# Kernel optimization log

Measured on AMD Instinct MI355X. Metric: run time of the kernel, lower is better.

Reference implementation:

```python
import jax, jax.numpy as jnp
import numpy as np
from jax import lax

ITER = 10
SMOOTH = 1.0


def _max_pool3(x):
    # 3x3 max pool, stride 1, pad 1 (torch pads with -inf for max pool)
    return lax.reduce_window(x, -np.inf, lax.max,
                             window_dimensions=(1, 1, 3, 3),
                             window_strides=(1, 1, 1, 1),
                             padding=((0, 0), (0, 0), (1, 1), (1, 1)))


def soft_skeletonize(x, thresh_width=ITER):
    def body(i, x):
        min_pool_x = -_max_pool3(-x)
        contour = jax.nn.relu(_max_pool3(min_pool_x) - min_pool_x)
        return jax.nn.relu(x - contour)
    return lax.fori_loop(0, thresh_width, body, x)


def setup_inputs() -> dict:
    key = jax.random.key(0)
    k1, k2 = jax.random.split(key)
    shape = (32, 2, 512, 512)
    y_pred = jax.random.uniform(k1, shape, dtype=jnp.float32)
    y_true = jax.random.uniform(k2, shape, dtype=jnp.float32)
    return {"y_pred": y_pred, "y_true": y_true}


def reference(y_pred, y_true):
    skel_pred = soft_skeletonize(y_pred, ITER)
    skel_true = soft_skeletonize(y_true, ITER)
    tprec = (jnp.sum((skel_pred * y_true)[:, 1:]) + SMOOTH) / (jnp.sum(skel_pred[:, 1:]) + SMOOTH)
    tsens = (jnp.sum((skel_true * y_pred)[:, 1:]) + SMOOTH) / (jnp.sum(skel_true[:, 1:]) + SMOOTH)
    cl_dice = 1.0 - 2.0 * (tprec * tsens) / (tprec + tsens)
    return cl_dice
```

## Files before the change

kernel.cpp:

```cpp
#include <hip/hip_runtime.h>

#define IMG 512
#define HW (IMG * IMG)
#define NB 32
#define NIMG 64
#define BAND 32
#define NBAND (IMG / BAND)
#define NSTG 5
#define HALO (2 * NSTG)
#define T0OFF 20
#define NSTEP 36
#define INF __builtin_inff()

static __device__ __forceinline__ float dpp_from_prev(float v, float ident) {
    return __int_as_float(__builtin_amdgcn_update_dpp(
        __float_as_int(ident), __float_as_int(v), 0x138, 0xF, 0xF, false));
}
static __device__ __forceinline__ float dpp_from_next(float v, float ident) {
    return __int_as_float(__builtin_amdgcn_update_dpp(
        __float_as_int(ident), __float_as_int(v), 0x130, 0xF, 0xF, false));
}

struct Row { float4 a, b; };

static __device__ __forceinline__ float min3f(float a, float b, float c) { return fminf(fminf(a, b), c); }
static __device__ __forceinline__ float max3f(float a, float b, float c) { return fmaxf(fmaxf(a, b), c); }

static __device__ __forceinline__ Row splat(float v) {
    Row r;
    r.a = make_float4(v, v, v, v);
    r.b = make_float4(v, v, v, v);
    return r;
}

static __device__ __forceinline__ Row rmin3(const Row& x, const Row& y, const Row& z) {
    Row o;
    const float* px = (const float*)&x;
    const float* py = (const float*)&y;
    const float* pz = (const float*)&z;
    float* po = (float*)&o;
#pragma unroll
    for (int i = 0; i < 8; ++i) po[i] = min3f(px[i], py[i], pz[i]);
    return o;
}

static __device__ __forceinline__ Row rmax3(const Row& x, const Row& y, const Row& z) {
    Row o;
    const float* px = (const float*)&x;
    const float* py = (const float*)&y;
    const float* pz = (const float*)&z;
    float* po = (float*)&o;
#pragma unroll
    for (int i = 0; i < 8; ++i) po[i] = max3f(px[i], py[i], pz[i]);
    return o;
}

static __device__ __forceinline__ Row hmin3(const Row& v) {
    float shl = dpp_from_prev(v.b.w, INF);
    float shr = dpp_from_next(v.a.x, INF);
    Row o;
    o.a.x = min3f(shl,   v.a.x, v.a.y);
    o.a.y = min3f(v.a.x, v.a.y, v.a.z);
    o.a.z = min3f(v.a.y, v.a.z, v.a.w);
    o.a.w = min3f(v.a.z, v.a.w, v.b.x);
    o.b.x = min3f(v.a.w, v.b.x, v.b.y);
    o.b.y = min3f(v.b.x, v.b.y, v.b.z);
    o.b.z = min3f(v.b.y, v.b.z, v.b.w);
    o.b.w = min3f(v.b.z, v.b.w, shr);
    return o;
}

static __device__ __forceinline__ Row hmax3(const Row& v) {
    float shl = dpp_from_prev(v.b.w, -INF);
    float shr = dpp_from_next(v.a.x, -INF);
    Row o;
    o.a.x = max3f(shl,   v.a.x, v.a.y);
    o.a.y = max3f(v.a.x, v.a.y, v.a.z);
    o.a.z = max3f(v.a.y, v.a.z, v.a.w);
    o.a.w = max3f(v.a.z, v.a.w, v.b.x);
    o.b.x = max3f(v.a.w, v.b.x, v.b.y);
    o.b.y = max3f(v.b.x, v.b.y, v.b.z);
    o.b.z = max3f(v.b.y, v.b.z, v.b.w);
    o.b.w = max3f(v.b.z, v.b.w, shr);
    return o;
}

static __device__ __forceinline__ Row relu_out(const Row& x, const Row& mp, const Row& mn) {
    Row o;
    const float* px = (const float*)&x;
    const float* pp = (const float*)&mp;
    const float* pm = (const float*)&mn;
    float* po = (float*)&o;
#pragma unroll
    for (int i = 0; i < 8; ++i) {
        float d = pp[i] - pm[i];
        po[i] = __builtin_amdgcn_fmed3f(0.f, px[i], px[i] - d);
    }
    return o;
}

static __device__ __forceinline__ Row load_row_clamped(const float* __restrict__ p,
                                                       int r, int lane) {
    const int rc = min(max(r, 0), IMG - 1);
    const float4* q = (const float4*)(p + (size_t)rc * IMG + lane * 8);
    Row o;
    o.a = q[0];
    o.b = q[1];
    return o;
}

template <bool EDGE>
static __device__ __forceinline__ void step2(Row (&x)[2], Row (&mn)[2],
                                             Row& in0, Row& in1, int t) {
    Row vmin0 = rmin3(x[0], x[1], in0);
    Row vmin1 = rmin3(x[1], in0, in1);
    Row mna = hmin3(vmin0);
    Row mnb = hmin3(vmin1);
    if (EDGE) {
        if ((unsigned)(t - 1) >= IMG) mna = splat(-INF);
        if ((unsigned)t >= IMG) mnb = splat(-INF);
    }
    Row vmax0 = rmax3(mn[0], mn[1], mna);
    Row vmax1 = rmax3(mn[1], mna, mnb);
    Row mp0 = hmax3(vmax0);
    Row mp1 = hmax3(vmax1);
    Row out0 = relu_out(x[0], mp0, mn[1]);
    Row out1 = relu_out(x[1], mp1, mna);
    if (EDGE) {
        if ((unsigned)(t - 2) >= IMG) out0 = splat(INF);
        if ((unsigned)(t - 1) >= IMG) out1 = splat(INF);
    }
    x[0] = in0;  x[1] = in1;
    mn[0] = mna; mn[1] = mnb;
    in0 = out0;  in1 = out1;
}

template <bool EDGE>
static __device__ __forceinline__ void pipe(const float* __restrict__ src,
                                            const float* __restrict__ wp,
                                            float4 (*ring)[2][128],
                                            int B, int lane, int wid,
                                            float& s_prod, float& s_val) {
    Row x[NSTG][2], mn[NSTG][2];
#pragma unroll
    for (int j = 0; j < NSTG; ++j) {
        x[j][0] = splat(INF);   x[j][1] = splat(INF);
        mn[j][0] = splat(-INF); mn[j][1] = splat(-INF);
    }
    const int t0 = B - T0OFF;
    Row pre0 = splat(0.f), pre1 = splat(0.f);
    if (wid == 0) {
        pre0 = load_row_clamped(src, t0, lane);
        pre1 = load_row_clamped(src, t0 + 1, lane);
    }
#pragma unroll 1
    for (int k = 0; k < NSTEP; ++k) {
        const int t = t0 + 2 * k;
        if (wid == 0) {
            Row nxt0 = load_row_clamped(src, t + 2, lane);
            Row nxt1 = load_row_clamped(src, t + 3, lane);
            Row in0 = pre0, in1 = pre1;
            if (EDGE) {
                if ((unsigned)t >= IMG) in0 = splat(INF);
                if ((unsigned)(t + 1) >= IMG) in1 = splat(INF);
            }
#pragma unroll
            for (int j = 0; j < NSTG; ++j)
                step2<EDGE>(x[j], mn[j], in0, in1, t - 2 * j);
            float4* r0 = &ring[k & 1][0][0];
            r0[lane * 2] = in0.a;
            r0[lane * 2 + 1] = in0.b;
            float4* r1 = &ring[k & 1][1][0];
            r1[lane * 2] = in1.a;
            r1[lane * 2 + 1] = in1.b;
            pre0 = nxt0;
            pre1 = nxt1;
        }
        __syncthreads();
        if (wid == 1) {
            const int u = t - HALO;
            const int v = u - HALO;
            const bool inband = (unsigned)(v - B) < BAND;
            Row w0, w1;
            if (inband) {
                const float4* q0 = (const float4*)(wp + (size_t)v * IMG + lane * 8);
                w0.a = q0[0]; w0.b = q0[1];
                const float4* q1 = (const float4*)(wp + (size_t)(v + 1) * IMG + lane * 8);
                w1.a = q1[0]; w1.b = q1[1];
            }
            const float4* r0 = &ring[k & 1][0][0];
            Row in0; in0.a = r0[lane * 2]; in0.b = r0[lane * 2 + 1];
            const float4* r1 = &ring[k & 1][1][0];
            Row in1; in1.a = r1[lane * 2]; in1.b = r1[lane * 2 + 1];
#pragma unroll
            for (int j = 0; j < NSTG; ++j)
                step2<EDGE>(x[j], mn[j], in0, in1, u - 2 * j);
            if (inband) {
                const float* p0 = (const float*)&in0;
                const float* p1 = (const float*)&in1;
                const float* q0 = (const float*)&w0;
                const float* q1 = (const float*)&w1;
#pragma unroll
                for (int i = 0; i < 8; ++i) {
                    s_prod += p0[i] * q0[i] + p1[i] * q1[i];
                    s_val += p0[i] + p1[i];
                }
            }
        }
    }
}

__global__ __launch_bounds__(128, 1) void skel10_pipe(const float* __restrict__ yp,
                                                      const float* __restrict__ yt,
                                                      double* __restrict__ acc) {
    __shared__ float4 ring[2][2][128];
    const int blk = blockIdx.x;
    const int img = blk >> 4, band = blk & (NBAND - 1);
    const float* src = (img < NB) ? yp + (size_t)(2 * img + 1) * HW
                                  : yt + (size_t)(2 * (img - NB) + 1) * HW;
    const float* wp = (img < NB) ? yt + (size_t)(2 * img + 1) * HW
                                 : yp + (size_t)(2 * (img - NB) + 1) * HW;
    const int lane = threadIdx.x & 63;
    const int wid = threadIdx.x >> 6;
    const int B = band * BAND;

    float s_prod = 0.f, s_val = 0.f;
    if (band == 0 || band == NBAND - 1)
        pipe<true>(src, wp, ring, B, lane, wid, s_prod, s_val);
    else
        pipe<false>(src, wp, ring, B, lane, wid, s_prod, s_val);

    if (wid == 1) {
#pragma unroll
        for (int off = 32; off; off >>= 1) {
            s_prod += __shfl_down(s_prod, off);
            s_val += __shfl_down(s_val, off);
        }
        if (lane == 0) {
            const int base = (img < NB) ? 0 : 2;
            atomicAdd(&acc[base], (double)s_prod);
            atomicAdd(&acc[base + 1], (double)s_val);
        }
    }
}

__global__ void finalize(const double* __restrict__ acc, float* __restrict__ out) {
    double tprec = (acc[0] + 1.0) / (acc[1] + 1.0);
    double tsens = (acc[2] + 1.0) / (acc[3] + 1.0);
    out[0] = (float)(1.0 - 2.0 * (tprec * tsens) / (tprec + tsens));
}

extern "C" void kernel_launch(void* const* d_in, const int* in_sizes, int n_in,
                              void* d_out, int out_size, void* d_ws, size_t ws_size,
                              hipStream_t stream) {
    (void)in_sizes; (void)n_in; (void)out_size; (void)ws_size;
    const float* yp = (const float*)d_in[0];
    const float* yt = (const float*)d_in[1];
    float* out = (float*)d_out;

    double* acc = (double*)d_ws;
    hipMemsetAsync(acc, 0, 4 * sizeof(double), stream);

    const int grid = NIMG * NBAND;
    skel10_pipe<<<grid, 128, 0, stream>>>(yp, yt, acc);
    finalize<<<1, 1, 0, stream>>>(acc, out);
}
```

Before: 268.4 us.

## Process four rows per barrier and fuse finalize via last-block counter

The producer/consumer wavefront pipeline now handles four rows per iteration instead of two, with a larger shared ring, so the number of __syncthreads barriers per band is halved. The separate finalize kernel is removed; the last block to finish, found with an atomic counter and threadfences, computes the clDice result. This removes one kernel launch and half the barrier stalls, at the cost of more registers for prefetched rows and serialized atomic reads at the end.

```diff
diff --git a/kernel.cpp b/kernel.cpp
--- a/kernel.cpp
+++ b/kernel.cpp
@@ -6,10 +6,11 @@
 #define NIMG 64
 #define BAND 32
 #define NBAND (IMG / BAND)
+#define NBLK (NIMG * NBAND)
 #define NSTG 5
 #define HALO (2 * NSTG)
 #define T0OFF 20
-#define NSTEP 36
+#define NSTEP2 18
 #define INF __builtin_inff()
 
 static __device__ __forceinline__ float dpp_from_prev(float v, float ident) {
@@ -138,7 +139,7 @@
 template <bool EDGE>
 static __device__ __forceinline__ void pipe(const float* __restrict__ src,
                                             const float* __restrict__ wp,
-                                            float4 (*ring)[2][128],
+                                            float4 (*ring)[4][128],
                                             int B, int lane, int wid,
                                             float& s_prod, float& s_val) {
     Row x[NSTG][2], mn[NSTG][2];
@@ -148,17 +149,21 @@
         mn[j][0] = splat(-INF); mn[j][1] = splat(-INF);
     }
     const int t0 = B - T0OFF;
-    Row pre0 = splat(0.f), pre1 = splat(0.f);
+    Row pre0 = splat(0.f), pre1 = splat(0.f), pre2 = splat(0.f), pre3 = splat(0.f);
     if (wid == 0) {
         pre0 = load_row_clamped(src, t0, lane);
         pre1 = load_row_clamped(src, t0 + 1, lane);
+        pre2 = load_row_clamped(src, t0 + 2, lane);
+        pre3 = load_row_clamped(src, t0 + 3, lane);
     }
 #pragma unroll 1
-    for (int k = 0; k < NSTEP; ++k) {
-        const int t = t0 + 2 * k;
+    for (int k = 0; k < NSTEP2; ++k) {
+        const int t = t0 + 4 * k;
         if (wid == 0) {
-            Row nxt0 = load_row_clamped(src, t + 2, lane);
-            Row nxt1 = load_row_clamped(src, t + 3, lane);
+            Row nxt0 = load_row_clamped(src, t + 4, lane);
+            Row nxt1 = load_row_clamped(src, t + 5, lane);
+            Row nxt2 = load_row_clamped(src, t + 6, lane);
+            Row nxt3 = load_row_clamped(src, t + 7, lane);
             Row in0 = pre0, in1 = pre1;
             if (EDGE) {
                 if ((unsigned)t >= IMG) in0 = splat(INF);
@@ -167,35 +172,45 @@
 #pragma unroll
             for (int j = 0; j < NSTG; ++j)
                 step2<EDGE>(x[j], mn[j], in0, in1, t - 2 * j);
-            float4* r0 = &ring[k & 1][0][0];
-            r0[lane * 2] = in0.a;
-            r0[lane * 2 + 1] = in0.b;
-            float4* r1 = &ring[k & 1][1][0];
-            r1[lane * 2] = in1.a;
-            r1[lane * 2 + 1] = in1.b;
-            pre0 = nxt0;
-            pre1 = nxt1;
+            ring[k & 1][0][lane * 2] = in0.a;
+            ring[k & 1][0][lane * 2 + 1] = in0.b;
+            ring[k & 1][1][lane * 2] = in1.a;
+            ring[k & 1][1][lane * 2 + 1] = in1.b;
+            Row in2 = pre2, in3 = pre3;
+            if (EDGE) {
+                if ((unsigned)(t + 2) >= IMG) in2 = splat(INF);
+                if ((unsigned)(t + 3) >= IMG) in3 = splat(INF);
+            }
+#pragma unroll
+            for (int j = 0; j < NSTG; ++j)
+                step2<EDGE>(x[j], mn[j], in2, in3, t + 2 - 2 * j);
+            ring[k & 1][2][lane * 2] = in2.a;
+            ring[k & 1][2][lane * 2 + 1] = in2.b;
+            ring[k & 1][3][lane * 2] = in3.a;
+            ring[k & 1][3][lane * 2 + 1] = in3.b;
+            pre0 = nxt0; pre1 = nxt1; pre2 = nxt2; pre3 = nxt3;
         }
         __syncthreads();
         if (wid == 1) {
-            const int u = t - HALO;
-            const int v = u - HALO;
-            const bool inband = (unsigned)(v - B) < BAND;
+            const int uA = t - HALO;
+            const int vA = uA - HALO;
+            const bool inbA = (unsigned)(vA - B) < BAND;
             Row w0, w1;
-            if (inband) {
-                const float4* q0 = (const float4*)(wp + (size_t)v * IMG + lane * 8);
+            if (inbA) {
+                const float4* q0 = (const float4*)(wp + (size_t)vA * IMG + lane * 8);
                 w0.a = q0[0]; w0.b = q0[1];
-                const float4* q1 = (const float4*)(wp + (size_t)(v + 1) * IMG + lane * 8);
+                const float4* q1 = (const float4*)(wp + (size_t)(vA + 1) * IMG + lane * 8);
                 w1.a = q1[0]; w1.b = q1[1];
             }
-            const float4* r0 = &ring[k & 1][0][0];
-            Row in0; in0.a = r0[lane * 2]; in0.b = r0[lane * 2 + 1];
-            const float4* r1 = &ring[k & 1][1][0];
-            Row in1; in1.a = r1[lane * 2]; in1.b = r1[lane * 2 + 1];
+            Row in0, in1;
+            in0.a = ring[k & 1][0][lane * 2];
+            in0.b = ring[k & 1][0][lane * 2 + 1];
+            in1.a = ring[k & 1][1][lane * 2];
+            in1.b = ring[k & 1][1][lane * 2 + 1];
 #pragma unroll
             for (int j = 0; j < NSTG; ++j)
-                step2<EDGE>(x[j], mn[j], in0, in1, u - 2 * j);
-            if (inband) {
+                step2<EDGE>(x[j], mn[j], in0, in1, uA - 2 * j);
+            if (inbA) {
                 const float* p0 = (const float*)&in0;
                 const float* p1 = (const float*)&in1;
                 const float* q0 = (const float*)&w0;
@@ -206,14 +221,44 @@
                     s_val += p0[i] + p1[i];
                 }
             }
+            const int vB = vA + 2;
+            const bool inbB = (unsigned)(vB - B) < BAND;
+            Row w2, w3;
+            if (inbB) {
+                const float4* q2 = (const float4*)(wp + (size_t)vB * IMG + lane * 8);
+                w2.a = q2[0]; w2.b = q2[1];
+                const float4* q3 = (const float4*)(wp + (size_t)(vB + 1) * IMG + lane * 8);
+                w3.a = q3[0]; w3.b = q3[1];
+            }
+            Row in2, in3;
+            in2.a = ring[k & 1][2][lane * 2];
+            in2.b = ring[k & 1][2][lane * 2 + 1];
+            in3.a = ring[k & 1][3][lane * 2];
+            in3.b = ring[k & 1][3][lane * 2 + 1];
+#pragma unroll
+            for (int j = 0; j < NSTG; ++j)
+                step2<EDGE>(x[j], mn[j], in2, in3, uA + 2 - 2 * j);
+            if (inbB) {
+                const float* p2 = (const float*)&in2;
+                const float* p3 = (const float*)&in3;
+                const float* q2 = (const float*)&w2;
+                const float* q3 = (const float*)&w3;
+#pragma unroll
+                for (int i = 0; i < 8; ++i) {
+                    s_prod += p2[i] * q2[i] + p3[i] * q3[i];
+                    s_val += p2[i] + p3[i];
+                }
+            }
         }
     }
 }
 
 __global__ __launch_bounds__(128, 1) void skel10_pipe(const float* __restrict__ yp,
                                                       const float* __restrict__ yt,
-                                                      double* __restrict__ acc) {
-    __shared__ float4 ring[2][2][128];
+                                                      double* __restrict__ acc,
+                                                      unsigned* __restrict__ ctr,
+                                                      float* __restrict__ out) {
+    __shared__ float4 ring[2][4][128];
     const int blk = blockIdx.x;
     const int img = blk >> 4, band = blk & (NBAND - 1);
     const float* src = (img < NB) ? yp + (size_t)(2 * img + 1) * HW
@@ -240,14 +285,20 @@
             const int base = (img < NB) ? 0 : 2;
             atomicAdd(&acc[base], (double)s_prod);
             atomicAdd(&acc[base + 1], (double)s_val);
+            __threadfence();
+            unsigned old = atomicAdd(ctr, 1u);
+            if (old == NBLK - 1) {
+                __threadfence();
+                double a0 = atomicAdd(&acc[0], 0.0);
+                double a1 = atomicAdd(&acc[1], 0.0);
+                double a2 = atomicAdd(&acc[2], 0.0);
+                double a3 = atomicAdd(&acc[3], 0.0);
+                double tprec = (a0 + 1.0) / (a1 + 1.0);
+                double tsens = (a2 + 1.0) / (a3 + 1.0);
+                out[0] = (float)(1.0 - 2.0 * (tprec * tsens) / (tprec + tsens));
+            }
         }
     }
-}
-
-__global__ void finalize(const double* __restrict__ acc, float* __restrict__ out) {
-    double tprec = (acc[0] + 1.0) / (acc[1] + 1.0);
-    double tsens = (acc[2] + 1.0) / (acc[3] + 1.0);
-    out[0] = (float)(1.0 - 2.0 * (tprec * tsens) / (tprec + tsens));
 }
 
 extern "C" void kernel_launch(void* const* d_in, const int* in_sizes, int n_in,
@@ -259,9 +310,8 @@
     float* out = (float*)d_out;
 
     double* acc = (double*)d_ws;
-    hipMemsetAsync(acc, 0, 4 * sizeof(double), stream);
-
-    const int grid = NIMG * NBAND;
-    skel10_pipe<<<grid, 128, 0, stream>>>(yp, yt, acc);
-    finalize<<<1, 1, 0, stream>>>(acc, out);
-}
+    unsigned* ctr = (unsigned*)(acc + 4);
+    hipMemsetAsync(acc, 0, 4 * sizeof(double) + sizeof(unsigned), stream);
+
+    skel10_pipe<<<NBLK, 128, 0, stream>>>(yp, yt, acc, ctr, out);
+}
```

Measured after the change: 270.3 us. About the same (+0.7%).
